# Kernel optimization log

Hardware: AMD Instinct MI355X
Metric: run time of the kernel (lower is better)

## Reference

```python
import jax, jax.numpy as jnp
import numpy as np


def rational_hat(points, centers, radius):
    # points: [B, P, 2], centers: [K, 2], radius: [1]
    # L1 distance of each point to each center: [B, P, K]
    norm = jnp.abs(points[:, :, None, :] - centers[None, None, :, :]).sum(-1)
    r = jnp.abs(radius[0])
    val = 1.0 / (1.0 + norm) - 1.0 / (1.0 + jnp.abs(r - norm))
    return val.sum(axis=1)  # [B, K]


def setup_inputs() -> dict:
    key = jax.random.key(0)
    k1, k2, k3, k4, k5 = jax.random.split(key, 5)
    B, N0, N1, N2, K = 32, 20000, 10000, 10000, 64
    return {
        "beta_0_up": jax.random.uniform(k1, (B, N0, 2), dtype=jnp.float32),
        "beta_0_down": jax.random.uniform(k2, (B, N0, 2), dtype=jnp.float32),
        "beta0_ext": jax.random.uniform(k3, (B, N1, 2), dtype=jnp.float32),
        "beta1_ext": jax.random.uniform(k4, (B, N2, 2), dtype=jnp.float32),
        "centers": jax.random.uniform(k5, (K, 2), dtype=jnp.float32),
        "radius": jnp.full((1,), 0.1, dtype=jnp.float32),
    }


def reference(beta_0_up, beta_0_down, beta0_ext, beta1_ext, centers, radius):
    x0, y0 = beta0_ext[..., 0], beta0_ext[..., 1]
    x1, y1 = beta1_ext[..., 0], beta1_ext[..., 1]
    b0_1st = jnp.stack([x0, 1.0 - x0], axis=-1)  # [B, N1, 2]
    b0_2nd = jnp.stack([y0, 1.0 - y0], axis=-1)
    b1_1st = jnp.stack([x1, 1.0 - x1], axis=-1)  # [B, N2, 2]
    b1_2nd = jnp.stack([y1, 1.0 - y1], axis=-1)
    ph_down = jnp.concatenate([beta_0_down, b0_1st, b1_1st], axis=1)  # [B, P, 2]
    ph_up = jnp.concatenate([beta_0_up, b0_2nd, b1_2nd], axis=1)
    up_out = rational_hat(ph_up, centers, radius)    # [B, K]
    down_out = rational_hat(ph_down, centers, radius)
    tpl = -((up_out - down_out) ** 2).sum()
    x = jnp.concatenate([up_out, down_out], axis=1)  # [B, 2K]
    return (x, tpl)
```

## Files before the change

kernel.cpp:

```cpp
#include <hip/hip_runtime.h>

#define NB 32
#define N0 20000
#define N1 10000
#define N2 10000
#define NP 40000
#define NK 64
#define TILES 625
#define CHUNKS 8
#define KC 16

__global__ __launch_bounds__(256) void hat_kernel(
    const float* __restrict__ up0, const float* __restrict__ down0,
    const float* __restrict__ ext0, const float* __restrict__ ext1,
    const float* __restrict__ centers, const float* __restrict__ radius,
    float* __restrict__ out)
{
    const int lane  = threadIdx.x & 63;
    const int wave  = threadIdx.x >> 6;
    const int b     = blockIdx.y;
    const int side  = blockIdx.z >> 2;
    const int cc    = blockIdx.z & 3;
    const int cbase = cc * KC;

    float cx[KC], cy[KC];
    #pragma unroll
    for (int k = 0; k < KC; ++k) {
        cx[k] = centers[2*(cbase+k)];
        cy[k] = centers[2*(cbase+k)+1];
    }
    const float r  = fabsf(radius[0]);
    const float r1 = 1.0f + r;

    const float2* base0 = (const float2*)((side == 0 ? up0 : down0) + (size_t)b * (N0*2));
    const float2* e0    = (const float2*)(ext0 + (size_t)b * (N1*2));
    const float2* e1    = (const float2*)(ext1 + (size_t)b * (N2*2));

    float acc[KC];
    #pragma unroll
    for (int k = 0; k < KC; ++k) acc[k] = 0.f;

    for (int t = blockIdx.x*4 + wave; t < TILES; t += CHUNKS*4) {
        const int p = t*64 + lane;
        float px, py;
        if (p < N0) {
            float2 v = base0[p];
            px = v.x; py = v.y;
        } else if (p < N0 + N1) {
            float2 v = e0[p - N0];
            float vv = (side == 0) ? v.y : v.x;
            px = vv; py = 1.0f - vv;
        } else {
            float2 v = e1[p - (N0 + N1)];
            float vv = (side == 0) ? v.y : v.x;
            px = vv; py = 1.0f - vv;
        }

        #pragma unroll
        for (int k = 0; k < KC; ++k) {
            const float t1 = px - cx[k];
            const float t2 = py - cy[k];
            const float n  = fabsf(t1) + fabsf(t2);
            const float u  = 1.0f + n;
            const float rn = r1 - u;
            const float bb = 1.0f + fabsf(rn);
            const float rc = __builtin_amdgcn_rcpf(u * bb);
            acc[k] = fmaf(bb - u, rc, acc[k]);
        }
    }

    {
        #pragma unroll
        for (int k = 0; k < 8; ++k) {
            const bool hi = lane & 32;
            const float send = hi ? acc[k]   : acc[k+8];
            const float keep = hi ? acc[k+8] : acc[k];
            acc[k] = keep + __shfl_xor(send, 32, 64);
        }
        #pragma unroll
        for (int k = 0; k < 4; ++k) {
            const bool hi = lane & 16;
            const float send = hi ? acc[k]   : acc[k+4];
            const float keep = hi ? acc[k+4] : acc[k];
            acc[k] = keep + __shfl_xor(send, 16, 64);
        }
        #pragma unroll
        for (int k = 0; k < 2; ++k) {
            const bool hi = lane & 8;
            const float send = hi ? acc[k]   : acc[k+2];
            const float keep = hi ? acc[k+2] : acc[k];
            acc[k] = keep + __shfl_xor(send, 8, 64);
        }
        {
            const bool hi = lane & 4;
            const float send = hi ? acc[0] : acc[1];
            const float keep = hi ? acc[1] : acc[0];
            acc[0] = keep + __shfl_xor(send, 4, 64);
        }
        acc[0] += __shfl_xor(acc[0], 2, 64);
        acc[0] += __shfl_xor(acc[0], 1, 64);
    }
    if ((lane & 3) == 0) {
        atomicAdd(&out[b*128 + side*64 + cbase + (lane >> 2)], acc[0]);
    }
}

__global__ __launch_bounds__(256) void tpl_kernel(float* __restrict__ out)
{
    __shared__ float red[256];
    float s = 0.f;
    for (int i = threadIdx.x; i < NB*NK; i += 256) {
        const int b = i >> 6, k = i & 63;
        const float d = out[b*128 + k] - out[b*128 + 64 + k];
        s = fmaf(d, d, s);
    }
    red[threadIdx.x] = s;
    __syncthreads();
    for (int w = 128; w > 0; w >>= 1) {
        if (threadIdx.x < w) red[threadIdx.x] += red[threadIdx.x + w];
        __syncthreads();
    }
    if (threadIdx.x == 0) out[NB*2*NK] = -red[0];
}

extern "C" void kernel_launch(void* const* d_in, const int* in_sizes, int n_in,
                              void* d_out, int out_size, void* d_ws, size_t ws_size,
                              hipStream_t stream) {
    const float* up0     = (const float*)d_in[0];
    const float* down0   = (const float*)d_in[1];
    const float* ext0    = (const float*)d_in[2];
    const float* ext1    = (const float*)d_in[3];
    const float* centers = (const float*)d_in[4];
    const float* radius  = (const float*)d_in[5];
    float* out = (float*)d_out;

    hipMemsetAsync(out, 0, NB * 2 * NK * sizeof(float), stream);

    dim3 grid(CHUNKS, NB, 8);
    hat_kernel<<<grid, 256, 0, stream>>>(up0, down0, ext0, ext1, centers, radius, out);
    tpl_kernel<<<1, 256, 0, stream>>>(out);
}
```

Before: 126.2 us.

## Rotate L1 distance to max form, pack two points per lane with float2 math

After: 127.5 us. No clear change (+1.0%).

```diff
diff --git a/kernel.cpp b/kernel.cpp
--- a/kernel.cpp
+++ b/kernel.cpp
@@ -1,107 +1,133 @@
 #include <hip/hip_runtime.h>
+
+typedef float v2f __attribute__((ext_vector_type(2)));
 
 #define NB 32
 #define N0 20000
 #define N1 10000
 #define N2 10000
-#define NP 40000
-#define NK 64
-#define TILES 625
-#define CHUNKS 8
-#define KC 16
+#define NPTS 40000
+#define NTILES 313
+#define KC 8
+#define TCHUNKS 4
+#define SENT 3.0e4f
 
-__global__ __launch_bounds__(256) void hat_kernel(
+__global__ __launch_bounds__(256, 8) void hat_kernel(
     const float* __restrict__ up0, const float* __restrict__ down0,
     const float* __restrict__ ext0, const float* __restrict__ ext1,
     const float* __restrict__ centers, const float* __restrict__ radius,
     float* __restrict__ out)
 {
-    const int lane  = threadIdx.x & 63;
-    const int wave  = threadIdx.x >> 6;
-    const int b     = blockIdx.y;
-    const int side  = blockIdx.z >> 2;
-    const int cc    = blockIdx.z & 3;
-    const int cbase = cc * KC;
+    const int tid    = threadIdx.x;
+    const int lane   = tid & 63;
+    const int wave   = tid >> 6;
+    const int bid    = blockIdx.x;
+    const int tchunk = bid & 3;
+    const int cc     = (bid >> 2) & 7;
+    const int side   = (bid >> 5) & 1;
+    const int b      = bid >> 6;
+    const int cbase  = cc * KC;
 
-    float cx[KC], cy[KC];
+    const float r = fabsf(radius[0]);
+
+    v2f nuc[KC], nvc[KC];
     #pragma unroll
     for (int k = 0; k < KC; ++k) {
-        cx[k] = centers[2*(cbase+k)];
-        cy[k] = centers[2*(cbase+k)+1];
+        const float cx = centers[2*(cbase+k)];
+        const float cy = centers[2*(cbase+k)+1];
+        nuc[k] = (v2f){-(cx + cy), -(cx + cy)};
+        nvc[k] = (v2f){-(cx - cy), -(cx - cy)};
     }
-    const float r  = fabsf(radius[0]);
-    const float r1 = 1.0f + r;
 
-    const float2* base0 = (const float2*)((side == 0 ? up0 : down0) + (size_t)b * (N0*2));
-    const float2* e0    = (const float2*)(ext0 + (size_t)b * (N1*2));
-    const float2* e1    = (const float2*)(ext1 + (size_t)b * (N2*2));
+    const float4* base0 = (const float4*)((side == 0 ? up0 : down0) + (size_t)b * (N0*2));
+    const float4* e0f   = (const float4*)(ext0 + (size_t)b * (N1*2));
+    const float4* e1f   = (const float4*)(ext1 + (size_t)b * (N2*2));
 
-    float acc[KC];
+    v2f acc[KC];
     #pragma unroll
-    for (int k = 0; k < KC; ++k) acc[k] = 0.f;
+    for (int k = 0; k < KC; ++k) acc[k] = (v2f){0.f, 0.f};
 
-    for (int t = blockIdx.x*4 + wave; t < TILES; t += CHUNKS*4) {
-        const int p = t*64 + lane;
-        float px, py;
-        if (p < N0) {
-            float2 v = base0[p];
-            px = v.x; py = v.y;
-        } else if (p < N0 + N1) {
-            float2 v = e0[p - N0];
-            float vv = (side == 0) ? v.y : v.x;
-            px = vv; py = 1.0f - vv;
+    const v2f one2 = (v2f){1.f, 1.f};
+
+    for (int t = tchunk*4 + wave; t < NTILES; t += TCHUNKS*4) {
+        const int i = t*64 + lane;
+        v2f u_, v_;
+        if (i < N0/2) {
+            const float4 q = base0[i];
+            u_ = (v2f){q.x + q.y, q.z + q.w};
+            v_ = (v2f){q.x - q.y, q.z - q.w};
+        } else if (i < (N0 + N1)/2) {
+            const float4 q = e0f[i - N0/2];
+            const float vv0 = (side == 0) ? q.y : q.x;
+            const float vv1 = (side == 0) ? q.w : q.z;
+            u_ = one2;
+            v_ = (v2f){2.f*vv0 - 1.f, 2.f*vv1 - 1.f};
+        } else if (i < NPTS/2) {
+            const float4 q = e1f[i - (N0 + N1)/2];
+            const float vv0 = (side == 0) ? q.y : q.x;
+            const float vv1 = (side == 0) ? q.w : q.z;
+            u_ = one2;
+            v_ = (v2f){2.f*vv0 - 1.f, 2.f*vv1 - 1.f};
         } else {
-            float2 v = e1[p - (N0 + N1)];
-            float vv = (side == 0) ? v.y : v.x;
-            px = vv; py = 1.0f - vv;
+            u_ = (v2f){SENT, SENT};
+            v_ = (v2f){0.f, 0.f};
         }
 
         #pragma unroll
         for (int k = 0; k < KC; ++k) {
-            const float t1 = px - cx[k];
-            const float t2 = py - cy[k];
-            const float n  = fabsf(t1) + fabsf(t2);
-            const float u  = 1.0f + n;
-            const float rn = r1 - u;
-            const float bb = 1.0f + fabsf(rn);
-            const float rc = __builtin_amdgcn_rcpf(u * bb);
-            acc[k] = fmaf(bb - u, rc, acc[k]);
+            const v2f du = u_ + nuc[k];
+            const v2f dv = v_ + nvc[k];
+            const float tt0 = fmaxf(fabsf(du.x), fabsf(dv.x));
+            const float tt1 = fmaxf(fabsf(du.y), fabsf(dv.y));
+            const v2f tt = (v2f){tt0, tt1};
+            const v2f d1 = tt + one2;
+            const float rn0 = r - tt0;
+            const float rn1 = r - tt1;
+            const v2f d2 = (v2f){1.f + fabsf(rn0), 1.f + fabsf(rn1)};
+            const v2f dd  = d1 * d2;
+            const v2f num = d2 - d1;
+            const v2f rc  = (v2f){__builtin_amdgcn_rcpf(dd.x),
+                                  __builtin_amdgcn_rcpf(dd.y)};
+            acc[k] = __builtin_elementwise_fma(num, rc, acc[k]);
         }
     }
 
+    float a1[KC];
+    #pragma unroll
+    for (int k = 0; k < KC; ++k) a1[k] = acc[k].x + acc[k].y;
+
     {
         #pragma unroll
-        for (int k = 0; k < 8; ++k) {
+        for (int k = 0; k < 4; ++k) {
             const bool hi = lane & 32;
-            const float send = hi ? acc[k]   : acc[k+8];
-            const float keep = hi ? acc[k+8] : acc[k];
-            acc[k] = keep + __shfl_xor(send, 32, 64);
-        }
-        #pragma unroll
-        for (int k = 0; k < 4; ++k) {
-            const bool hi = lane & 16;
-            const float send = hi ? acc[k]   : acc[k+4];
-            const float keep = hi ? acc[k+4] : acc[k];
-            acc[k] = keep + __shfl_xor(send, 16, 64);
+            const float send = hi ? a1[k]   : a1[k+4];
+            const float keep = hi ? a1[k+4] : a1[k];
+            a1[k] = keep + __shfl_xor(send, 32, 64);
         }
         #pragma unroll
         for (int k = 0; k < 2; ++k) {
-            const bool hi = lane & 8;
-            const float send = hi ? acc[k]   : acc[k+2];
-            const float keep = hi ? acc[k+2] : acc[k];
-            acc[k] = keep + __shfl_xor(send, 8, 64);
+            const bool hi = lane & 16;
+            const float send = hi ? a1[k]   : a1[k+2];
+            const float keep = hi ? a1[k+2] : a1[k];
+            a1[k] = keep + __shfl_xor(send, 16, 64);
         }
         {
-            const bool hi = lane & 4;
-            const float send = hi ? acc[0] : acc[1];
-            const float keep = hi ? acc[1] : acc[0];
-            acc[0] = keep + __shfl_xor(send, 4, 64);
+            const bool hi = lane & 8;
+            const float send = hi ? a1[0] : a1[1];
+            const float keep = hi ? a1[1] : a1[0];
+            a1[0] = keep + __shfl_xor(send, 8, 64);
         }
-        acc[0] += __shfl_xor(acc[0], 2, 64);
-        acc[0] += __shfl_xor(acc[0], 1, 64);
+        a1[0] += __shfl_xor(a1[0], 4, 64);
+        a1[0] += __shfl_xor(a1[0], 2, 64);
+        a1[0] += __shfl_xor(a1[0], 1, 64);
     }
-    if ((lane & 3) == 0) {
-        atomicAdd(&out[b*128 + side*64 + cbase + (lane >> 2)], acc[0]);
+
+    __shared__ float red[4 * KC];
+    if ((lane & 7) == 0) red[wave * KC + (lane >> 3)] = a1[0];
+    __syncthreads();
+    if (tid < KC) {
+        const float s = red[tid] + red[KC + tid] + red[2*KC + tid] + red[3*KC + tid];
+        atomicAdd(&out[b*128 + side*64 + cbase + tid], s);
     }
 }
 
@@ -109,7 +135,7 @@
 {
     __shared__ float red[256];
     float s = 0.f;
-    for (int i = threadIdx.x; i < NB*NK; i += 256) {
+    for (int i = threadIdx.x; i < NB*64; i += 256) {
         const int b = i >> 6, k = i & 63;
         const float d = out[b*128 + k] - out[b*128 + 64 + k];
         s = fmaf(d, d, s);
@@ -120,7 +146,7 @@
         if (threadIdx.x < w) red[threadIdx.x] += red[threadIdx.x + w];
         __syncthreads();
     }
-    if (threadIdx.x == 0) out[NB*2*NK] = -red[0];
+    if (threadIdx.x == 0) out[NB*128] = -red[0];
 }
 
 extern "C" void kernel_launch(void* const* d_in, const int* in_sizes, int n_in,
@@ -134,9 +160,9 @@
     const float* radius  = (const float*)d_in[5];
     float* out = (float*)d_out;
 
-    hipMemsetAsync(out, 0, NB * 2 * NK * sizeof(float), stream);
+    hipMemsetAsync(out, 0, NB * 128 * sizeof(float), stream);
 
-    dim3 grid(CHUNKS, NB, 8);
-    hat_kernel<<<grid, 256, 0, stream>>>(up0, down0, ext0, ext1, centers, radius, out);
+    hat_kernel<<<dim3(NB * 2 * 8 * TCHUNKS), dim3(256), 0, stream>>>(
+        up0, down0, ext0, ext1, centers, radius, out);
     tpl_kernel<<<1, 256, 0, stream>>>(out);
 }
```
